# Kernel tuning notes

Hardware: AMD Instinct MI355X
Metric: run time of the kernel (lower is better)

The kernel has to match this reference:

```python
import jax, jax.numpy as jnp
import numpy as np

B_ = 2; L_ = 4096; D_MODEL = 1024; D_INNER = 2048; D_STATE = 128
N_HEADS = 32; HEADDIM = 64; D_CONV = 4; CHUNK = 64
CONV_DIM = D_INNER + 2 * D_STATE
EPS = 1e-5


def silu(x):
    return x * jax.nn.sigmoid(x)


def segsum(x):
    # x: (..., T) -> (..., T, T) stable segment sums; exp() gives 1-semiseparable matrix
    T = x.shape[-1]
    xe = jnp.broadcast_to(x[..., None], x.shape + (T,))  # (..., T, T)
    lower = jnp.tril(jnp.ones((T, T), bool), -1)
    xs = jnp.cumsum(jnp.where(lower, xe, 0.0), axis=-2)
    incl = jnp.tril(jnp.ones((T, T), bool), 0)
    return jnp.where(incl, xs, -jnp.inf)


def ssd(x, A, Bm, Cm):
    # x: (b, l, h, p); A: (b, l, h); Bm/Cm: (b, l, n) (single shared head, as in module)
    b, l, h, p = x.shape
    c = l // CHUNK
    x = x.reshape(b, c, CHUNK, h, p)
    A = A.reshape(b, c, CHUNK, h).transpose(0, 3, 1, 2)  # (b, h, c, l)
    Bm = Bm.reshape(b, c, CHUNK, D_STATE)
    Cm = Cm.reshape(b, c, CHUNK, D_STATE)
    A_cumsum = jnp.cumsum(A, axis=-1)                    # (b, h, c, l)
    Lmat = jnp.exp(segsum(A))                            # (b, h, c, l, l)
    # intra-chunk (diagonal blocks)
    Y_diag = jnp.einsum('bcln,bcsn,bhcls,bcshp->bclhp', Cm, Bm, Lmat, x)
    # per-chunk states
    decay_states = jnp.exp(A_cumsum[:, :, :, -1:] - A_cumsum)  # (b, h, c, l)
    states = jnp.einsum('bcln,bhcl,bclhp->bchpn', Bm, decay_states, x)
    init = jnp.zeros_like(states[:, :1])
    states = jnp.concatenate([init, states], axis=1)     # (b, c+1, h, p, n)
    A_last = jnp.pad(A_cumsum[:, :, :, -1], ((0, 0), (0, 0), (1, 0)))  # (b, h, c+1)
    decay_chunk = jnp.exp(segsum(A_last))                # (b, h, c+1, c+1)
    new_states = jnp.einsum('bhzc,bchpn->bzhpn', decay_chunk, states)
    states_prev = new_states[:, :-1]                     # (b, c, h, p, n)
    state_decay_out = jnp.exp(A_cumsum)
    Y_off = jnp.einsum('bcln,bchpn,bhcl->bclhp', Cm, states_prev, state_decay_out)
    return (Y_diag + Y_off).reshape(b, l, h, p)


def setup_inputs() -> dict:
    key = jax.random.key(0)
    ks = jax.random.split(key, 9)
    u = jax.random.normal(ks[0], (B_, L_, D_MODEL), jnp.float32)
    W_in = jax.random.normal(ks[1], (2 * D_INNER + 2 * D_STATE + N_HEADS, D_MODEL), jnp.float32) * (D_MODEL ** -0.5)
    conv_w = jax.random.normal(ks[2], (CONV_DIM, 1, D_CONV), jnp.float32) * 0.2
    conv_b = jax.random.normal(ks[3], (CONV_DIM,), jnp.float32) * 0.02
    dt_bias = jax.random.normal(ks[4], (N_HEADS,), jnp.float32) * 0.1
    A_log = jnp.log(jax.random.uniform(ks[5], (N_HEADS,), jnp.float32, 1.0, 16.0))
    D_param = jax.random.normal(ks[6], (N_HEADS,), jnp.float32) * 0.5
    norm_w = jnp.ones((D_INNER,), jnp.float32)
    W_out = jax.random.normal(ks[7], (D_MODEL, D_INNER), jnp.float32) * (D_INNER ** -0.5)
    return dict(u=u, W_in=W_in, conv_w=conv_w, conv_b=conv_b, dt_bias=dt_bias,
                A_log=A_log, D_param=D_param, norm_w=norm_w, W_out=W_out)


def mamba_forward(u, W_in, conv_w, conv_b, dt_bias, A_log, D_param, norm_w, W_out):
    b, l, _ = u.shape
    zxbcdt = u @ W_in.T                                  # (b, l, 2*di+2*ds+h)
    z = zxbcdt[..., :D_INNER]
    xBC = zxbcdt[..., D_INNER:D_INNER + CONV_DIM]
    dt = zxbcdt[..., D_INNER + CONV_DIM:]
    dt = jax.nn.softplus(dt + dt_bias)                   # (b, l, h)
    # causal depthwise conv1d
    xc = jnp.transpose(xBC, (0, 2, 1))                   # (b, conv_dim, l)
    xc = jax.lax.conv_general_dilated(xc, conv_w, (1,), [(D_CONV - 1, 0)],
                                      feature_group_count=CONV_DIM,
                                      dimension_numbers=('NCH', 'OIH', 'NCH'))
    xc = xc + conv_b[None, :, None]
    xBC = silu(jnp.transpose(xc, (0, 2, 1)))             # (b, l, conv_dim)
    x = xBC[..., :D_INNER]
    Bc = xBC[..., D_INNER:D_INNER + D_STATE]
    Cc = xBC[..., D_INNER + D_STATE:]
    x = x.reshape(b, l, N_HEADS, HEADDIM)
    A = -jnp.exp(A_log)                                  # (h,)
    Y = ssd(x * dt[..., None], A * dt, Bc, Cc)           # (b, l, h, p)
    y = Y + x * D_param[:, None]
    y = y.reshape(b, l, D_INNER)
    # gated RMSNorm
    y = y * silu(z)
    y = y * jax.lax.rsqrt(jnp.mean(y * y, axis=-1, keepdims=True) + EPS) * norm_w
    return y @ W_out.T


def reference(u, W_in, conv_w, conv_b, dt_bias, A_log, D_param, norm_w, W_out):
    return mamba_forward(u, W_in, conv_w, conv_b, dt_bias, A_log, D_param, norm_w, W_out)
```

## Files before the change

kernel.cpp:

```cpp
#include <hip/hip_runtime.h>
#include <hip/hip_bf16.h>
#include <math.h>

#define B_    2
#define L_    4096
#define DM    1024
#define DI    2048
#define DS    128
#define NH    32
#define HD    64
#define CHUNK 64
#define NC    (L_/CHUNK)
#define CD    (DI + 2*DS)
#define ROWS  (B_*L_)
#define NOUT  (2*DI + 2*DS + NH)
#define NPAD2 4608

typedef __attribute__((ext_vector_type(4))) float f32x4;
typedef __attribute__((ext_vector_type(8))) __bf16 bf16x8;
typedef __attribute__((ext_vector_type(4))) short s16x4;
typedef __attribute__((ext_vector_type(8))) short s16x8;

__global__ __launch_bounds__(256) void k_f32_to_bf16(const float* __restrict__ s, __bf16* __restrict__ d, int n4) {
    int i = blockIdx.x * 256 + threadIdx.x;
    if (i < n4) {
        f32x4 v = *(const f32x4*)(s + (size_t)i * 4);
        s16x4 o;
#pragma unroll
        for (int q = 0; q < 4; q++) o[q] = __builtin_bit_cast(short, (__bf16)v[q]);
        *(s16x4*)(d + (size_t)i * 4) = o;
    }
}

__global__ __launch_bounds__(256) void k_convert_pad(const float* __restrict__ s, __bf16* __restrict__ d, int nsrc4, int ndst4) {
    int i = blockIdx.x * 256 + threadIdx.x;
    if (i < ndst4) {
        s16x4 o = {0, 0, 0, 0};
        if (i < nsrc4) {
            f32x4 v = *(const f32x4*)(s + (size_t)i * 4);
#pragma unroll
            for (int q = 0; q < 4; q++) o[q] = __builtin_bit_cast(short, (__bf16)v[q]);
        }
        *(s16x4*)(d + (size_t)i * 4) = o;
    }
}

__device__ __forceinline__ void stage_half(const __bf16* __restrict__ G, int ldg, int grow0, int kt,
                                           char* lds, int ldsoff, int tid, int wave) {
#pragma unroll
    for (int issue = 0; issue < 2; issue++) {
        int o   = issue * 8192 + tid * 16;
        int row = o >> 7;
        int cb  = (o & 127) ^ ((row & 7) << 4);
        const __bf16* src = G + (size_t)(grow0 + row) * ldg + kt + (cb >> 1);
        char* ldsbase = lds + ldsoff + issue * 8192 + wave * 1024;
        __builtin_amdgcn_global_load_lds((const __attribute__((address_space(1))) void*)src,
                                         (__attribute__((address_space(3))) void*)ldsbase,
                                         16, 0, 0);
    }
}

__device__ __forceinline__ bf16x8 rdfrag(const char* lds, int ldsoff, int r, int ks, int lane) {
    int logical = r * 128 + ks * 64 + ((lane >> 4) << 4);
    int phys    = logical ^ ((r & 7) << 4);
    return *(const bf16x8*)(lds + ldsoff + phys);
}

#define MFMA_CLUSTER(AF, BF, ACC)                                                         \
    __builtin_amdgcn_s_setprio(1);                                                       \
    _Pragma("unroll")                                                                    \
    for (int fm = 0; fm < 4; fm++)                                                       \
        _Pragma("unroll")                                                                \
        for (int fn = 0; fn < 2; fn++)                                                   \
            _Pragma("unroll")                                                            \
            for (int ks = 0; ks < 2; ks++)                                               \
                ACC[fm][fn] = __builtin_amdgcn_mfma_f32_16x16x32_bf16(AF[fm][ks], BF[fn][ks], ACC[fm][fn], 0, 0, 0); \
    __builtin_amdgcn_s_setprio(0);

__device__ __forceinline__ void gemm256_core(const __bf16* __restrict__ Ag, const __bf16* __restrict__ Bg,
                                             int K, int m0, int n0, char* lds, f32x4 acc[4][4][2]) {
    const int tid = threadIdx.x, wave = tid >> 6, lane = tid & 63;
    const int wmq = wave >> 2, wnq = wave & 3, lrow = lane & 15;
    const int KT = K >> 6;
    auto Ahalf = [](int p, int mh) { return p * 65536 + mh * 16384; };
    auto Bhalf = [](int p, int nh) { return p * 65536 + 32768 + nh * 16384; };

    stage_half(Ag, K, m0,       0, lds, Ahalf(0, 0), tid, wave);
    stage_half(Bg, K, n0,       0, lds, Bhalf(0, 0), tid, wave);
    stage_half(Bg, K, n0 + 128, 0, lds, Bhalf(0, 1), tid, wave);
    stage_half(Ag, K, m0 + 128, 0, lds, Ahalf(0, 1), tid, wave);
    asm volatile("s_waitcnt vmcnt(0)" ::: "memory");
    __builtin_amdgcn_s_barrier();

    bf16x8 ra[4][2], rb[2][2], rb2[2][2];
#pragma unroll
    for (int fm = 0; fm < 4; fm++)
#pragma unroll
        for (int ks = 0; ks < 2; ks++)
            ra[fm][ks] = rdfrag(lds, Ahalf(0, 0), wmq * 64 + fm * 16 + lrow, ks, lane);
#pragma unroll
    for (int fn = 0; fn < 2; fn++)
#pragma unroll
        for (int ks = 0; ks < 2; ks++)
            rb[fn][ks] = rdfrag(lds, Bhalf(0, 0), wnq * 32 + fn * 16 + lrow, ks, lane);

    for (int t = 0; t < KT; t++) {
        const int p = t & 1, pn = p ^ 1, kn = (t + 1) << 6;
        const bool dsg = (t + 1 < KT);
        if (dsg) {
            stage_half(Ag, K, m0, kn, lds, Ahalf(pn, 0), tid, wave);
            stage_half(Bg, K, n0, kn, lds, Bhalf(pn, 0), tid, wave);
        }
#pragma unroll
        for (int fn = 0; fn < 2; fn++)
#pragma unroll
            for (int ks = 0; ks < 2; ks++)
                rb2[fn][ks] = rdfrag(lds, Bhalf(p, 1), wnq * 32 + fn * 16 + lrow, ks, lane);
        MFMA_CLUSTER(ra, rb, acc[0]);
        if (dsg) {
            stage_half(Bg, K, n0 + 128, kn, lds, Bhalf(pn, 1), tid, wave);
            stage_half(Ag, K, m0 + 128, kn, lds, Ahalf(pn, 1), tid, wave);
        }
        MFMA_CLUSTER(ra, rb2, acc[1]);
#pragma unroll
        for (int fm = 0; fm < 4; fm++)
#pragma unroll
            for (int ks = 0; ks < 2; ks++)
                ra[fm][ks] = rdfrag(lds, Ahalf(p, 1), wmq * 64 + fm * 16 + lrow, ks, lane);
        MFMA_CLUSTER(ra, rb2, acc[2]);
        MFMA_CLUSTER(ra, rb, acc[3]);
        asm volatile("s_waitcnt vmcnt(0)" ::: "memory");
        __builtin_amdgcn_s_barrier();
        if (dsg) {
#pragma unroll
            for (int fm = 0; fm < 4; fm++)
#pragma unroll
                for (int ks = 0; ks < 2; ks++)
                    ra[fm][ks] = rdfrag(lds, Ahalf(pn, 0), wmq * 64 + fm * 16 + lrow, ks, lane);
#pragma unroll
            for (int fn = 0; fn < 2; fn++)
#pragma unroll
                for (int ks = 0; ks < 2; ks++)
                    rb[fn][ks] = rdfrag(lds, Bhalf(pn, 0), wnq * 32 + fn * 16 + lrow, ks, lane);
        }
    }
}

__device__ __forceinline__ void gemm256x128_core(const __bf16* __restrict__ Ag, const __bf16* __restrict__ Bg,
                                                 int K, int m0, int n0, char* lds, f32x4 acc[8][2]) {
    const int tid = threadIdx.x, wave = tid >> 6, lane = tid & 63;
    const int wmq = wave >> 2, wnq = wave & 3, lrow = lane & 15;
    const int KT = K >> 6;
    const int aoff = wmq * 16384;

    auto stage_tile = [&](int t, int p) {
        const int kt = t << 6;
        stage_half(Ag, K, m0,       kt, lds, p * 49152,         tid, wave);
        stage_half(Ag, K, m0 + 128, kt, lds, p * 49152 + 16384, tid, wave);
        stage_half(Bg, K, n0,       kt, lds, p * 49152 + 32768, tid, wave);
    };
    stage_tile(0, 0);
    asm volatile("s_waitcnt vmcnt(0)" ::: "memory");
    __builtin_amdgcn_s_barrier();

    bf16x8 ra[4][2], rb[2][2];
#pragma unroll
    for (int fm = 0; fm < 4; fm++)
#pragma unroll
        for (int ks = 0; ks < 2; ks++)
            ra[fm][ks] = rdfrag(lds, aoff, fm * 16 + lrow, ks, lane);
#pragma unroll
    for (int fn = 0; fn < 2; fn++)
#pragma unroll
        for (int ks = 0; ks < 2; ks++)
            rb[fn][ks] = rdfrag(lds, 32768, wnq * 32 + fn * 16 + lrow, ks, lane);

    for (int t = 0; t < KT; t++) {
        const int p = t & 1, pn = p ^ 1;
        const bool dsg = (t + 1 < KT);
        if (dsg) {
            stage_half(Ag, K, m0,       (t + 1) << 6, lds, pn * 49152,         tid, wave);
            stage_half(Ag, K, m0 + 128, (t + 1) << 6, lds, pn * 49152 + 16384, tid, wave);
        }
        {
            f32x4 (*a0)[2] = &acc[0];
            MFMA_CLUSTER(ra, rb, a0);
        }
#pragma unroll
        for (int fm = 0; fm < 4; fm++)
#pragma unroll
            for (int ks = 0; ks < 2; ks++)
                ra[fm][ks] = rdfrag(lds, p * 49152 + aoff, 64 + fm * 16 + lrow, ks, lane);
        if (dsg) stage_half(Bg, K, n0, (t + 1) << 6, lds, pn * 49152 + 32768, tid, wave);
        {
            f32x4 (*a1)[2] = &acc[4];
            MFMA_CLUSTER(ra, rb, a1);
        }
        asm volatile("s_waitcnt vmcnt(0)" ::: "memory");
        __builtin_amdgcn_s_barrier();
        if (dsg) {
#pragma unroll
            for (int fm = 0; fm < 4; fm++)
#pragma unroll
                for (int ks = 0; ks < 2; ks++)
                    ra[fm][ks] = rdfrag(lds, pn * 49152 + aoff, fm * 16 + lrow, ks, lane);
#pragma unroll
            for (int fn = 0; fn < 2; fn++)
#pragma unroll
                for (int ks = 0; ks < 2; ks++)
                    rb[fn][ks] = rdfrag(lds, pn * 49152 + 32768, wnq * 32 + fn * 16 + lrow, ks, lane);
        }
    }
}

__global__ __launch_bounds__(512, 2) void k_gemm1(const __bf16* __restrict__ ubf, const __bf16* __restrict__ wibf,
                                                  __bf16* __restrict__ zbuf, __bf16* __restrict__ xbcraw,
                                                  float* __restrict__ dtbuf, const float* __restrict__ dt_bias) {
    extern __shared__ char lds[];
    f32x4 acc[4][4][2];
    f32x4 z4 = {0.f, 0.f, 0.f, 0.f};
#pragma unroll
    for (int q = 0; q < 4; q++)
#pragma unroll
        for (int i = 0; i < 4; i++)
#pragma unroll
            for (int j = 0; j < 2; j++) acc[q][i][j] = z4;

    int bid = blockIdx.x;
    int wg  = (bid & 7) * 72 + (bid >> 3);
    int m0  = (wg / 18) * 256;
    int n0  = (wg % 18) * 256;
    gemm256_core(ubf, wibf, DM, m0, n0, lds, acc);

    const int lane = threadIdx.x & 63, wave = threadIdx.x >> 6;
    const int wmq = wave >> 2, wnq = wave & 3;
#pragma unroll
    for (int q = 0; q < 4; q++) {
        const int mh = q >> 1, nh = (q & 1) ^ (q >> 1);
#pragma unroll
        for (int fm = 0; fm < 4; fm++) {
            const int gmb = m0 + mh * 128 + wmq * 64 + fm * 16 + ((lane >> 4) << 2);
#pragma unroll
            for (int fn = 0; fn < 2; fn++) {
                const int gn = n0 + nh * 128 + wnq * 32 + fn * 16 + (lane & 15);
                if (gn < DI) {
#pragma unroll
                    for (int r = 0; r < 4; r++)
                        zbuf[(size_t)(gmb + r) * DI + gn] = (__bf16)acc[q][fm][fn][r];
                } else if (gn < DI + CD) {
#pragma unroll
                    for (int r = 0; r < 4; r++)
                        xbcraw[(size_t)(gmb + r) * CD + (gn - DI)] = (__bf16)acc[q][fm][fn][r];
                } else if (gn < NOUT) {
                    const int hh = gn - (DI + CD);
                    const float bb = dt_bias[hh];
#pragma unroll
                    for (int r = 0; r < 4; r++) {
                        float x = acc[q][fm][fn][r] + bb;
                        float sp = (x > 20.f) ? x : log1pf(__expf(x));
                        dtbuf[(size_t)(gmb + r) * NH + hh] = sp;
                    }
                }
            }
        }
    }
}

__global__ __launch_bounds__(512, 2) void k_gemm2(const __bf16* __restrict__ ybf, const __bf16* __restrict__ wobf,
                                                  float* __restrict__ out) {
    extern __shared__ char lds[];
    f32x4 acc[8][2];
    f32x4 z4 = {0.f, 0.f, 0.f, 0.f};
#pragma unroll
    for (int i = 0; i < 8; i++)
#pragma unroll
        for (int j = 0; j < 2; j++) acc[i][j] = z4;

    int bid = blockIdx.x;
    int wg  = (bid & 7) * 32 + (bid >> 3);
    int m0  = (wg / 8) * 256;
    int n0  = (wg % 8) * 128;
    gemm256x128_core(ybf, wobf, DI, m0, n0, lds, acc);

    const int lane = threadIdx.x & 63, wave = threadIdx.x >> 6;
    const int wmq = wave >> 2, wnq = wave & 3;
#pragma unroll
    for (int fm = 0; fm < 8; fm++) {
        const int gmb = m0 + wmq * 128 + fm * 16 + ((lane >> 4) << 2);
#pragma unroll
        for (int fn = 0; fn < 2; fn++) {
            const int gn = n0 + wnq * 32 + fn * 16 + (lane & 15);
#pragma unroll
            for (int r = 0; r < 4; r++)
                out[(size_t)(gmb + r) * DM + gn] = acc[fm][fn][r];
        }
    }
}

__global__ __launch_bounds__(256) void k_conv(const __bf16* __restrict__ xbcraw, const float* __restrict__ conv_w,
                                              const float* __restrict__ conv_b, __bf16* __restrict__ xconv) {
    __shared__ float wsh[256 * 4];
    __shared__ float bsh[256];
    const int tid  = threadIdx.x;
    const int gsub = tid & 31;
    const int roct = tid >> 5;
    const int ch_base_blk = blockIdx.x * 256;
    *(f32x4*)&wsh[tid * 4] = *(const f32x4*)&conv_w[ch_base_blk * 4 + tid * 4];
    bsh[tid] = conv_b[ch_base_blk + tid];
    __syncthreads();

    const int ch0  = ch_base_blk + gsub * 8;
    const int row0 = (blockIdx.y * 8 + roct) * 8;
    const int l0   = row0 & (L_ - 1);
    const __bf16* src = xbcraw + (size_t)row0 * CD + ch0;

    s16x8 rr[11];
#pragma unroll
    for (int j = 0; j < 11; j++) {
        int ll = l0 - 3 + j;
        if (ll >= 0) rr[j] = *(const s16x8*)(src + (size_t)(j - 3) * CD);
        else         rr[j] = (s16x8){0, 0, 0, 0, 0, 0, 0, 0};
    }

    const int chl = gsub * 8;
    float w[8][4], bias[8];
#pragma unroll
    for (int j = 0; j < 8; j++) {
        bias[j] = bsh[chl + j];
#pragma unroll
        for (int k = 0; k < 4; k++) w[j][k] = wsh[(chl + j) * 4 + k];
    }

    __bf16* dst = xconv + (size_t)row0 * CD + ch0;
#pragma unroll
    for (int orow = 0; orow < 8; orow++) {
        float a[8];
#pragma unroll
        for (int j = 0; j < 8; j++) a[j] = bias[j];
#pragma unroll
        for (int k = 0; k < 4; k++) {
            s16x8 v = rr[orow + k];
#pragma unroll
            for (int j = 0; j < 8; j++)
                a[j] += w[j][k] * (float)__builtin_bit_cast(__bf16, (short)v[j]);
        }
        s16x8 o;
#pragma unroll
        for (int j = 0; j < 8; j++)
            o[j] = __builtin_bit_cast(short, (__bf16)(a[j] * __builtin_amdgcn_rcpf(1.f + __expf(-a[j]))));
        *(s16x8*)(dst + (size_t)orow * CD) = o;
    }
}

__global__ __launch_bounds__(256) void k_cbt(const __bf16* __restrict__ xconv, float* __restrict__ cbt) {
    const int c = blockIdx.x, b = blockIdx.y;
    const int tid = threadIdx.x, wv = tid >> 6, lane = tid & 63;
    const int lrow = lane & 15, lko = (lane >> 4) * 8;
    __shared__ __align__(16) __bf16 Csh[64 * 136];
    __shared__ __align__(16) __bf16 Bsh[64 * 136];
    const size_t rowbase = (size_t)b * L_ + c * CHUNK;
#pragma unroll
    for (int q = 0; q < 32; q++) {
        int i = q * 2 + (wv >> 1);
        int n = (wv & 1) * 64 + lane;
        const __bf16* base = xconv + (rowbase + i) * CD + DI;
        Bsh[i * 136 + n] = base[n];
        Csh[i * 136 + n] = base[DS + n];
    }
    __syncthreads();
    f32x4 acc[4];
    f32x4 z4 = {0.f, 0.f, 0.f, 0.f};
#pragma unroll
    for (int jt = 0; jt < 4; jt++) acc[jt] = z4;
#pragma unroll
    for (int ks = 0; ks < 4; ks++) {
        bf16x8 a = *(const bf16x8*)&Csh[(wv * 16 + lrow) * 136 + ks * 32 + lko];
#pragma unroll
        for (int jt = 0; jt < 4; jt++) {
            bf16x8 bb = *(const bf16x8*)&Bsh[(jt * 16 + lrow) * 136 + ks * 32 + lko];
            acc[jt] = __builtin_amdgcn_mfma_f32_16x16x32_bf16(a, bb, acc[jt], 0, 0, 0);
        }
    }
    float* o = cbt + (size_t)(b * NC + c) * 4096;
#pragma unroll
    for (int jt = 0; jt < 4; jt++)
#pragma unroll
        for (int r = 0; r < 4; r++) {
            int i = wv * 16 + (lane >> 4) * 4 + r;
            int j = jt * 16 + lrow;
            o[i * 64 + j] = acc[jt][r];
        }
}

__global__ __launch_bounds__(256) void k_ssd_a(const __bf16* __restrict__ xconv, const float* __restrict__ dtbuf,
                                               const float* __restrict__ cbt, const float* __restrict__ A_log,
                                               __bf16* __restrict__ ybuf, __bf16* __restrict__ states,
                                               float* __restrict__ asum, const float* __restrict__ D_param) {
    const int h = blockIdx.x, c = blockIdx.y, b = blockIdx.z;
    const int tid = threadIdx.x, wv = tid >> 6, lane = tid & 63;
    const int lrow = lane & 15, lko = (lane >> 4) * 8;
    __shared__ __align__(16) __bf16 xT[64 * 72];
    __shared__ __align__(16) __bf16 xsc[64 * 72];
    __shared__ __align__(16) __bf16 BT[128 * 72];
    __shared__ __align__(16) __bf16 Ms[64 * 72];
    __shared__ float dts[64], cum[64];

    const float Ah = -__expf(A_log[h]);
    const size_t rowbase = (size_t)b * L_ + c * CHUNK;

    float dtv = 0.f;
    if (wv == 0) { dtv = dtbuf[(rowbase + lane) * NH + h]; dts[lane] = dtv; }
#pragma unroll
    for (int q = 0; q < 16; q++) {
        int i = q * 4 + wv;
        xT[lane * 72 + i] = xconv[(rowbase + i) * CD + h * HD + lane];
    }
#pragma unroll
    for (int q = 0; q < 32; q++) {
        int i = q * 2 + (wv >> 1);
        int n = (wv & 1) * 64 + lane;
        BT[n * 72 + i] = xconv[(rowbase + i) * CD + DI + n];
    }
    if (wv == 0) {
        float v = Ah * dtv;
#pragma unroll
        for (int o = 1; o < 64; o <<= 1) { float t = __shfl_up(v, o); if (lane >= o) v += t; }
        cum[lane] = v;
        if (lane == 63) asum[(b * NC + c) * NH + h] = v;
    }
    __syncthreads();

    const float cum63 = cum[63];
    const float Dh = D_param[h];
    const float* cbt_bc = cbt + (size_t)(b * NC + c) * 4096;
#pragma unroll
    for (int q = 0; q < 16; q++) {
        int i = q * 4 + wv, j = lane;
        float cumi = cum[i];
        float m = 0.f;
        if (j <= i) m = cbt_bc[i * 64 + j] * __expf(cumi - cum[j]) * dts[j];
        if (j == i) m += Dh;
        Ms[i * 72 + j] = (__bf16)m;
        float dcfi = __expf(cum63 - cumi) * dts[i];
        xsc[lane * 72 + i] = (__bf16)((float)xT[lane * 72 + i] * dcfi);
    }
    __syncthreads();

    f32x4 z4 = {0.f, 0.f, 0.f, 0.f};
    {
        f32x4 accY[4];
#pragma unroll
        for (int pt = 0; pt < 4; pt++) accY[pt] = z4;
#pragma unroll
        for (int ks = 0; ks < 2; ks++) {
            bf16x8 a = *(const bf16x8*)&Ms[(wv * 16 + lrow) * 72 + ks * 32 + lko];
#pragma unroll
            for (int pt = 0; pt < 4; pt++) {
                bf16x8 bb = *(const bf16x8*)&xT[(pt * 16 + lrow) * 72 + ks * 32 + lko];
                accY[pt] = __builtin_amdgcn_mfma_f32_16x16x32_bf16(a, bb, accY[pt], 0, 0, 0);
            }
        }
#pragma unroll
        for (int pt = 0; pt < 4; pt++)
#pragma unroll
            for (int r = 0; r < 4; r++) {
                int i = wv * 16 + (lane >> 4) * 4 + r;
                int p = pt * 16 + lrow;
                ybuf[(rowbase + i) * DI + h * HD + p] = (__bf16)accY[pt][r];
            }
    }
    {
        f32x4 accS[8];
#pragma unroll
        for (int nt = 0; nt < 8; nt++) accS[nt] = z4;
#pragma unroll
        for (int ks = 0; ks < 2; ks++) {
            bf16x8 a = *(const bf16x8*)&xsc[(wv * 16 + lrow) * 72 + ks * 32 + lko];
#pragma unroll
            for (int nt = 0; nt < 8; nt++) {
                bf16x8 bb = *(const bf16x8*)&BT[(nt * 16 + lrow) * 72 + ks * 32 + lko];
                accS[nt] = __builtin_amdgcn_mfma_f32_16x16x32_bf16(a, bb, accS[nt], 0, 0, 0);
            }
        }
        __bf16* sp = states + ((size_t)(b * NC + c) * NH + h) * 8192;
#pragma unroll
        for (int nt = 0; nt < 8; nt++)
#pragma unroll
            for (int r = 0; r < 4; r++) {
                int p = wv * 16 + (lane >> 4) * 4 + r;
                int n = nt * 16 + lrow;
                sp[p * 128 + n] = (__bf16)accS[nt][r];
            }
    }
}

__global__ __launch_bounds__(256) void k_scan(__bf16* __restrict__ states, const float* __restrict__ asum) {
    const int seg = blockIdx.x, h = blockIdx.y, b = blockIdx.z;
    __shared__ float efs[NC];
    if (threadIdx.x < NC) efs[threadIdx.x] = __expf(asum[(b * NC + threadIdx.x) * NH + h]);
    __syncthreads();
    const int e0 = seg * 1024 + threadIdx.x * 4;
    __bf16* base = states + ((size_t)(b * NC) * NH + h) * 8192 + e0;
    const size_t cs = (size_t)NH * 8192;
    float S[4] = {0.f, 0.f, 0.f, 0.f};
    s16x4 r0 = *(const s16x4*)(base);
    s16x4 r1 = *(const s16x4*)(base + cs);
    s16x4 r2 = *(const s16x4*)(base + 2 * cs);
    s16x4 r3;
#define SCAN_STEP(RV, CC)                                                                  \
    {                                                                                      \
        s16x4 o; float e = efs[CC];                                                        \
        _Pragma("unroll")                                                                  \
        for (int q = 0; q < 4; q++) {                                                      \
            float t = (float)__builtin_bit_cast(__bf16, (short)RV[q]);                     \
            o[q] = __builtin_bit_cast(short, (__bf16)S[q]);                                \
            S[q] = e * S[q] + t;                                                           \
        }                                                                                  \
        *(s16x4*)(base + (size_t)(CC) * cs) = o;                                           \
    }
    for (int c = 0; c < NC; c += 4) {
        r3 = *(const s16x4*)(base + (size_t)(c + 3) * cs);
        SCAN_STEP(r0, c);
        if (c + 4 < NC) r0 = *(const s16x4*)(base + (size_t)(c + 4) * cs);
        SCAN_STEP(r1, c + 1);
        if (c + 5 < NC) r1 = *(const s16x4*)(base + (size_t)(c + 5) * cs);
        SCAN_STEP(r2, c + 2);
        if (c + 6 < NC) r2 = *(const s16x4*)(base + (size_t)(c + 6) * cs);
        SCAN_STEP(r3, c + 3);
    }
#undef SCAN_STEP
}

__global__ __launch_bounds__(256) void k_ssd_b(const __bf16* __restrict__ xconv, const float* __restrict__ dtbuf,
                                               const __bf16* __restrict__ states, const float* __restrict__ A_log,
                                               __bf16* __restrict__ ybuf) {
    const int h = blockIdx.x, c = blockIdx.y, b = blockIdx.z;
    const int tid = threadIdx.x, wv = tid >> 6, lane = tid & 63;
    const int lrow = lane & 15, lko = (lane >> 4) * 8;
    __shared__ __align__(16) __bf16 Csh[64 * 136];
    __shared__ __align__(16) __bf16 Sps[64 * 136];
    __shared__ float cum[64];

    const float Ah = -__expf(A_log[h]);
    const size_t rowbase = (size_t)b * L_ + c * CHUNK;
    const __bf16* sp = states + ((size_t)(b * NC + c) * NH + h) * 8192;
#pragma unroll
    for (int q = 0; q < 32; q++) {
        int i = q * 2 + (wv >> 1);
        int n = (wv & 1) * 64 + lane;
        Csh[i * 136 + n] = xconv[(rowbase + i) * CD + DI + DS + n];
        Sps[i * 136 + n] = sp[i * 128 + n];
    }
    if (wv == 0) {
        float v = Ah * dtbuf[(rowbase + lane) * NH + h];
#pragma unroll
        for (int o = 1; o < 64; o <<= 1) { float t = __shfl_up(v, o); if (lane >= o) v += t; }
        cum[lane] = v;
    }
    __syncthreads();

    f32x4 acc[4];
    f32x4 z4 = {0.f, 0.f, 0.f, 0.f};
#pragma unroll
    for (int pt = 0; pt < 4; pt++) acc[pt] = z4;
#pragma unroll
    for (int ks = 0; ks < 4; ks++) {
        bf16x8 a = *(const bf16x8*)&Csh[(wv * 16 + lrow) * 136 + ks * 32 + lko];
#pragma unroll
        for (int pt = 0; pt < 4; pt++) {
            bf16x8 bb = *(const bf16x8*)&Sps[(pt * 16 + lrow) * 136 + ks * 32 + lko];
            acc[pt] = __builtin_amdgcn_mfma_f32_16x16x32_bf16(a, bb, acc[pt], 0, 0, 0);
        }
    }
#pragma unroll
    for (int r = 0; r < 4; r++) {
        int i = wv * 16 + (lane >> 4) * 4 + r;
        float ef = __expf(cum[i]);
#pragma unroll
        for (int pt = 0; pt < 4; pt++) {
            size_t idx = (rowbase + i) * DI + h * HD + pt * 16 + lrow;
            float y0 = (float)ybuf[idx];
            ybuf[idx] = (__bf16)(y0 + ef * acc[pt][r]);
        }
    }
}

__global__ __launch_bounds__(256) void k_gate_norm(const __bf16* __restrict__ ybuf, const __bf16* __restrict__ zbuf,
                                                   const float* __restrict__ norm_w, __bf16* __restrict__ ybf) {
    const int r = blockIdx.x;
    const int tid = threadIdx.x;
    const int col0 = tid * 8;
    s16x8 y8 = *(const s16x8*)(ybuf + (size_t)r * DI + col0);
    s16x8 z8 = *(const s16x8*)(zbuf + (size_t)r * DI + col0);
    float v[8];
    float ss = 0.f;
#pragma unroll
    for (int q = 0; q < 8; q++) {
        float y = (float)__builtin_bit_cast(__bf16, (short)y8[q]);
        float z = (float)__builtin_bit_cast(__bf16, (short)z8[q]);
        float g = z * __builtin_amdgcn_rcpf(1.f + __expf(-z));
        v[q] = y * g;
        ss += v[q] * v[q];
    }
#pragma unroll
    for (int o = 32; o > 0; o >>= 1) ss += __shfl_down(ss, o);
    __shared__ float wsum[4];
    __shared__ float rmss;
    if ((tid & 63) == 0) wsum[tid >> 6] = ss;
    __syncthreads();
    if (tid == 0) {
        float t = wsum[0] + wsum[1] + wsum[2] + wsum[3];
        rmss = rsqrtf(t / (float)DI + 1e-5f);
    }
    __syncthreads();
    float rm = rmss;
    s16x8 o8;
#pragma unroll
    for (int q = 0; q < 8; q++)
        o8[q] = __builtin_bit_cast(short, (__bf16)(v[q] * rm * norm_w[col0 + q]));
    *(s16x8*)(ybf + (size_t)r * DI + col0) = o8;
}

extern "C" void kernel_launch(void* const* d_in, const int* in_sizes, int n_in,
                              void* d_out, int out_size, void* d_ws, size_t ws_size,
                              hipStream_t stream) {
    const float* u       = (const float*)d_in[0];
    const float* W_in    = (const float*)d_in[1];
    const float* conv_w  = (const float*)d_in[2];
    const float* conv_b  = (const float*)d_in[3];
    const float* dt_bias = (const float*)d_in[4];
    const float* A_log   = (const float*)d_in[5];
    const float* D_param = (const float*)d_in[6];
    const float* norm_w  = (const float*)d_in[7];
    const float* W_out   = (const float*)d_in[8];
    float* out = (float*)d_out;

    constexpr size_t OFF_WOBF  = 0;
    constexpr size_t OFF_ZBUF  = 4194304;
    constexpr size_t OFF_DT    = 37748736;
    constexpr size_t OFF_ASUM  = 38797312;
    constexpr size_t OFF_XCONV = 38813696;
    constexpr size_t OFF_CBT   = 76562432;
    constexpr size_t OFF_BIG   = 78659584;
    constexpr size_t NEED      = 145768448;
    if (ws_size < NEED) return;

    char* ws = (char*)d_ws;
    __bf16* wobf   = (__bf16*)(ws + OFF_WOBF);
    __bf16* zbuf   = (__bf16*)(ws + OFF_ZBUF);
    float*  dtbuf  = (float*) (ws + OFF_DT);
    float*  asum   = (float*) (ws + OFF_ASUM);
    __bf16* xconv  = (__bf16*)(ws + OFF_XCONV);
    float*  cbt    = (float*) (ws + OFF_CBT);
    __bf16* ubf    = (__bf16*)(ws + OFF_BIG);
    __bf16* wibf   = (__bf16*)(ws + OFF_BIG + 16777216);
    __bf16* xbcraw = (__bf16*)(ws + OFF_BIG + 16777216 + 9437184);
    __bf16* states = (__bf16*)(ws + OFF_BIG);
    __bf16* ybf    = (__bf16*)(ws + OFF_XCONV);
    __bf16* ybuf   = (__bf16*)d_out;

    (void)hipFuncSetAttribute((const void*)k_gemm1, hipFuncAttributeMaxDynamicSharedMemorySize, 131072);
    (void)hipFuncSetAttribute((const void*)k_gemm2, hipFuncAttributeMaxDynamicSharedMemorySize, 98304);

    k_f32_to_bf16<<<(ROWS * DM / 4 + 255) / 256, 256, 0, stream>>>(u, ubf, ROWS * DM / 4);
    k_convert_pad<<<(NPAD2 * DM / 4 + 255) / 256, 256, 0, stream>>>(W_in, wibf, NOUT * DM / 4, NPAD2 * DM / 4);
    k_f32_to_bf16<<<(DM * DI / 4 + 255) / 256, 256, 0, stream>>>(W_out, wobf, DM * DI / 4);

    k_gemm1<<<576, 512, 131072, stream>>>(ubf, wibf, zbuf, xbcraw, dtbuf, dt_bias);
    k_conv<<<dim3(9, 128), 256, 0, stream>>>(xbcraw, conv_w, conv_b, xconv);
    k_cbt<<<dim3(NC, B_), 256, 0, stream>>>(xconv, cbt);
    k_ssd_a<<<dim3(NH, NC, B_), 256, 0, stream>>>(xconv, dtbuf, cbt, A_log, ybuf, states, asum, D_param);
    k_scan<<<dim3(8, NH, B_), 256, 0, stream>>>(states, asum);
    k_ssd_b<<<dim3(NH, NC, B_), 256, 0, stream>>>(xconv, dtbuf, states, A_log, ybuf);
    k_gate_norm<<<ROWS, 256, 0, stream>>>(ybuf, zbuf, norm_w, ybf);
    k_gemm2<<<256, 512, 98304, stream>>>(ybf, wobf, out);
}
```

Measured before the change: 311.2 us.

## Rewrite in-projection GEMM main loop as an 8-phase ping-pong schedule

Replaces the double-buffered 256x256 GEMM core used by the input projection with an 8-phase schedule. Each phase interleaves LDS fragment reads, one global-to-LDS stage of a half tile, and one MFMA cluster, separated by barriers and partial vmcnt waits. Two K tiles are kept in flight, and the accumulator quadrant mapping changes to match. The aim is to spread memory traffic evenly across MFMA work and hide load latency, at the cost of many more barriers per K step.

```diff
diff --git a/kernel.cpp b/kernel.cpp
--- a/kernel.cpp
+++ b/kernel.cpp
@@ -77,73 +77,66 @@
                 ACC[fm][fn] = __builtin_amdgcn_mfma_f32_16x16x32_bf16(AF[fm][ks], BF[fn][ks], ACC[fm][fn], 0, 0, 0); \
     __builtin_amdgcn_s_setprio(0);
 
-__device__ __forceinline__ void gemm256_core(const __bf16* __restrict__ Ag, const __bf16* __restrict__ Bg,
-                                             int K, int m0, int n0, char* lds, f32x4 acc[4][4][2]) {
+#define RDA(SET, BUF, H)                                                                  \
+    _Pragma("unroll") for (int fm = 0; fm < 4; fm++)                                      \
+    _Pragma("unroll") for (int ks = 0; ks < 2; ks++)                                      \
+        SET[fm][ks] = rdfrag(lds, (BUF)*65536 + (H)*16384, wmq*64 + fm*16 + lrow, ks, lane);
+#define RDB(SET, BUF, H)                                                                  \
+    _Pragma("unroll") for (int fn = 0; fn < 2; fn++)                                      \
+    _Pragma("unroll") for (int ks = 0; ks < 2; ks++)                                      \
+        SET[fn][ks] = rdfrag(lds, (BUF)*65536 + 32768 + (H)*16384, wnq*32 + fn*16 + lrow, ks, lane);
+#define STA(BUF, H, KOFF) stage_half(Ag, K, m0 + (H)*128, (KOFF), lds, (BUF)*65536 + (H)*16384, tid, wave)
+#define STB(BUF, H, KOFF) stage_half(Bg, K, n0 + (H)*128, (KOFF), lds, (BUF)*65536 + 32768 + (H)*16384, tid, wave)
+#define BAR() __builtin_amdgcn_s_barrier()
+#define LGKM0() asm volatile("s_waitcnt lgkmcnt(0)" ::: "memory")
+#define VMW(N) asm volatile("s_waitcnt vmcnt(" #N ")" ::: "memory")
+
+__device__ __forceinline__ void gemm256_8ph(const __bf16* __restrict__ Ag, const __bf16* __restrict__ Bg,
+                                            int K, int m0, int n0, char* lds, f32x4 acc[4][4][2]) {
     const int tid = threadIdx.x, wave = tid >> 6, lane = tid & 63;
     const int wmq = wave >> 2, wnq = wave & 3, lrow = lane & 15;
     const int KT = K >> 6;
-    auto Ahalf = [](int p, int mh) { return p * 65536 + mh * 16384; };
-    auto Bhalf = [](int p, int nh) { return p * 65536 + 32768 + nh * 16384; };
-
-    stage_half(Ag, K, m0,       0, lds, Ahalf(0, 0), tid, wave);
-    stage_half(Bg, K, n0,       0, lds, Bhalf(0, 0), tid, wave);
-    stage_half(Bg, K, n0 + 128, 0, lds, Bhalf(0, 1), tid, wave);
-    stage_half(Ag, K, m0 + 128, 0, lds, Ahalf(0, 1), tid, wave);
-    asm volatile("s_waitcnt vmcnt(0)" ::: "memory");
-    __builtin_amdgcn_s_barrier();
-
-    bf16x8 ra[4][2], rb[2][2], rb2[2][2];
-#pragma unroll
-    for (int fm = 0; fm < 4; fm++)
-#pragma unroll
-        for (int ks = 0; ks < 2; ks++)
-            ra[fm][ks] = rdfrag(lds, Ahalf(0, 0), wmq * 64 + fm * 16 + lrow, ks, lane);
-#pragma unroll
-    for (int fn = 0; fn < 2; fn++)
-#pragma unroll
-        for (int ks = 0; ks < 2; ks++)
-            rb[fn][ks] = rdfrag(lds, Bhalf(0, 0), wnq * 32 + fn * 16 + lrow, ks, lane);
-
-    for (int t = 0; t < KT; t++) {
-        const int p = t & 1, pn = p ^ 1, kn = (t + 1) << 6;
-        const bool dsg = (t + 1 < KT);
-        if (dsg) {
-            stage_half(Ag, K, m0, kn, lds, Ahalf(pn, 0), tid, wave);
-            stage_half(Bg, K, n0, kn, lds, Bhalf(pn, 0), tid, wave);
-        }
-#pragma unroll
-        for (int fn = 0; fn < 2; fn++)
-#pragma unroll
-            for (int ks = 0; ks < 2; ks++)
-                rb2[fn][ks] = rdfrag(lds, Bhalf(p, 1), wnq * 32 + fn * 16 + lrow, ks, lane);
-        MFMA_CLUSTER(ra, rb, acc[0]);
-        if (dsg) {
-            stage_half(Bg, K, n0 + 128, kn, lds, Bhalf(pn, 1), tid, wave);
-            stage_half(Ag, K, m0 + 128, kn, lds, Ahalf(pn, 1), tid, wave);
-        }
-        MFMA_CLUSTER(ra, rb2, acc[1]);
-#pragma unroll
-        for (int fm = 0; fm < 4; fm++)
-#pragma unroll
-            for (int ks = 0; ks < 2; ks++)
-                ra[fm][ks] = rdfrag(lds, Ahalf(p, 1), wmq * 64 + fm * 16 + lrow, ks, lane);
-        MFMA_CLUSTER(ra, rb2, acc[2]);
-        MFMA_CLUSTER(ra, rb, acc[3]);
-        asm volatile("s_waitcnt vmcnt(0)" ::: "memory");
-        __builtin_amdgcn_s_barrier();
-        if (dsg) {
-#pragma unroll
-            for (int fm = 0; fm < 4; fm++)
-#pragma unroll
-                for (int ks = 0; ks < 2; ks++)
-                    ra[fm][ks] = rdfrag(lds, Ahalf(pn, 0), wmq * 64 + fm * 16 + lrow, ks, lane);
-#pragma unroll
-            for (int fn = 0; fn < 2; fn++)
-#pragma unroll
-                for (int ks = 0; ks < 2; ks++)
-                    rb[fn][ks] = rdfrag(lds, Bhalf(pn, 0), wnq * 32 + fn * 16 + lrow, ks, lane);
-        }
-    }
+    const int NB = (KT >> 1) - 1;
+
+    bf16x8 a0s[4][2], a1s[4][2], b0s[2][2], b1s[2][2];
+
+    STA(0, 0, 0);  STB(0, 0, 0);  STA(0, 1, 0);  STB(0, 1, 0);
+    STA(1, 0, 64); STB(1, 0, 64); STA(1, 1, 64); STB(1, 1, 64);
+    VMW(8); BAR();
+    RDA(a0s, 0, 0); RDB(b0s, 0, 0);
+    BAR(); LGKM0(); MFMA_CLUSTER(a0s, b0s, acc[2]); BAR();
+    RDA(a1s, 0, 1);
+    BAR(); LGKM0(); MFMA_CLUSTER(a1s, b0s, acc[3]); BAR();
+
+    for (int i = 0; i < NB; i++) {
+        const int k2 = (2 * i + 2) << 6, k3 = k2 + 64;
+        RDB(b1s, 0, 1); STB(0, 0, k2);
+        BAR(); LGKM0(); MFMA_CLUSTER(a0s, b1s, acc[0]); BAR();
+        STA(0, 0, k2);
+        BAR(); LGKM0(); MFMA_CLUSTER(a1s, b1s, acc[1]); VMW(4); BAR();
+        RDA(a0s, 1, 0); RDB(b0s, 1, 0); STA(0, 1, k2);
+        BAR(); LGKM0(); MFMA_CLUSTER(a0s, b0s, acc[2]); BAR();
+        RDA(a1s, 1, 1); STB(0, 1, k2);
+        BAR(); LGKM0(); MFMA_CLUSTER(a1s, b0s, acc[3]); BAR();
+        RDB(b1s, 1, 1); STB(1, 0, k3);
+        BAR(); LGKM0(); MFMA_CLUSTER(a0s, b1s, acc[0]); BAR();
+        STA(1, 0, k3);
+        BAR(); LGKM0(); MFMA_CLUSTER(a1s, b1s, acc[1]); VMW(4); BAR();
+        RDA(a0s, 0, 0); RDB(b0s, 0, 0); STA(1, 1, k3);
+        BAR(); LGKM0(); MFMA_CLUSTER(a0s, b0s, acc[2]); BAR();
+        RDA(a1s, 0, 1); STB(1, 1, k3);
+        BAR(); LGKM0(); MFMA_CLUSTER(a1s, b0s, acc[3]); BAR();
+    }
+    RDB(b1s, 0, 1);
+    BAR(); LGKM0(); MFMA_CLUSTER(a0s, b1s, acc[0]); BAR();
+    BAR(); LGKM0(); MFMA_CLUSTER(a1s, b1s, acc[1]); VMW(0); BAR();
+    RDA(a0s, 1, 0); RDB(b0s, 1, 0);
+    BAR(); LGKM0(); MFMA_CLUSTER(a0s, b0s, acc[2]); BAR();
+    RDA(a1s, 1, 1);
+    BAR(); LGKM0(); MFMA_CLUSTER(a1s, b0s, acc[3]); BAR();
+    RDB(b1s, 1, 1);
+    BAR(); LGKM0(); MFMA_CLUSTER(a0s, b1s, acc[0]); BAR();
+    LGKM0(); MFMA_CLUSTER(a1s, b1s, acc[1]);
 }
 
 __device__ __forceinline__ void gemm256x128_core(const __bf16* __restrict__ Ag, const __bf16* __restrict__ Bg,
@@ -230,13 +223,13 @@
     int wg  = (bid & 7) * 72 + (bid >> 3);
     int m0  = (wg / 18) * 256;
     int n0  = (wg % 18) * 256;
-    gemm256_core(ubf, wibf, DM, m0, n0, lds, acc);
+    gemm256_8ph(ubf, wibf, DM, m0, n0, lds, acc);
 
     const int lane = threadIdx.x & 63, wave = threadIdx.x >> 6;
     const int wmq = wave >> 2, wnq = wave & 3;
 #pragma unroll
-    for (int q = 0; q < 4; q++) {
-        const int mh = q >> 1, nh = (q & 1) ^ (q >> 1);
+    for (int j = 0; j < 4; j++) {
+        const int mh = j & 1, nh = 1 - (j >> 1);
 #pragma unroll
         for (int fm = 0; fm < 4; fm++) {
             const int gmb = m0 + mh * 128 + wmq * 64 + fm * 16 + ((lane >> 4) << 2);
@@ -246,17 +239,17 @@
                 if (gn < DI) {
 #pragma unroll
                     for (int r = 0; r < 4; r++)
-                        zbuf[(size_t)(gmb + r) * DI + gn] = (__bf16)acc[q][fm][fn][r];
+                        zbuf[(size_t)(gmb + r) * DI + gn] = (__bf16)acc[j][fm][fn][r];
                 } else if (gn < DI + CD) {
 #pragma unroll
                     for (int r = 0; r < 4; r++)
-                        xbcraw[(size_t)(gmb + r) * CD + (gn - DI)] = (__bf16)acc[q][fm][fn][r];
+                        xbcraw[(size_t)(gmb + r) * CD + (gn - DI)] = (__bf16)acc[j][fm][fn][r];
                 } else if (gn < NOUT) {
                     const int hh = gn - (DI + CD);
                     const float bb = dt_bias[hh];
 #pragma unroll
                     for (int r = 0; r < 4; r++) {
-                        float x = acc[q][fm][fn][r] + bb;
+                        float x = acc[j][fm][fn][r] + bb;
                         float sp = (x > 20.f) ? x : log1pf(__expf(x));
                         dtbuf[(size_t)(gmb + r) * NH + hh] = sp;
                     }
```

Result: slower. 475.2 us (+52.7%).

## Shrink gemm1 tile to 128x256 with single-buffered LDS and higher occupancy

Applied to the files above, without the earlier changes.

Replaces the double-buffered, software-pipelined 256x256 gemm1 core with a simpler single-buffered 128x256 tile. LDS use per block drops from 128KB to 48KB and the launch bound goes from 2 to 4 blocks per CU, so twice as many workgroups run with more resident per CU. The aim is to hide load latency through occupancy instead of explicit prefetch. The trade is that global loads are no longer overlapped with MFMA inside a block, each block now has two barriers per K step, and the smaller M tile gives less reuse of the B operand.

```diff
diff --git a/kernel.cpp b/kernel.cpp
--- a/kernel.cpp
+++ b/kernel.cpp
@@ -77,72 +77,41 @@
                 ACC[fm][fn] = __builtin_amdgcn_mfma_f32_16x16x32_bf16(AF[fm][ks], BF[fn][ks], ACC[fm][fn], 0, 0, 0); \
     __builtin_amdgcn_s_setprio(0);
 
-__device__ __forceinline__ void gemm256_core(const __bf16* __restrict__ Ag, const __bf16* __restrict__ Bg,
-                                             int K, int m0, int n0, char* lds, f32x4 acc[4][4][2]) {
+__device__ __forceinline__ void gemm128x256_core(const __bf16* __restrict__ Ag, const __bf16* __restrict__ Bg,
+                                                 int K, int m0, int n0, char* lds, f32x4 acc[4][4]) {
     const int tid = threadIdx.x, wave = tid >> 6, lane = tid & 63;
-    const int wmq = wave >> 2, wnq = wave & 3, lrow = lane & 15;
+    const int wm = wave >> 2, wn = wave & 3, lrow = lane & 15;
     const int KT = K >> 6;
-    auto Ahalf = [](int p, int mh) { return p * 65536 + mh * 16384; };
-    auto Bhalf = [](int p, int nh) { return p * 65536 + 32768 + nh * 16384; };
-
-    stage_half(Ag, K, m0,       0, lds, Ahalf(0, 0), tid, wave);
-    stage_half(Bg, K, n0,       0, lds, Bhalf(0, 0), tid, wave);
-    stage_half(Bg, K, n0 + 128, 0, lds, Bhalf(0, 1), tid, wave);
-    stage_half(Ag, K, m0 + 128, 0, lds, Ahalf(0, 1), tid, wave);
-    asm volatile("s_waitcnt vmcnt(0)" ::: "memory");
-    __builtin_amdgcn_s_barrier();
-
-    bf16x8 ra[4][2], rb[2][2], rb2[2][2];
-#pragma unroll
-    for (int fm = 0; fm < 4; fm++)
-#pragma unroll
-        for (int ks = 0; ks < 2; ks++)
-            ra[fm][ks] = rdfrag(lds, Ahalf(0, 0), wmq * 64 + fm * 16 + lrow, ks, lane);
-#pragma unroll
-    for (int fn = 0; fn < 2; fn++)
-#pragma unroll
-        for (int ks = 0; ks < 2; ks++)
-            rb[fn][ks] = rdfrag(lds, Bhalf(0, 0), wnq * 32 + fn * 16 + lrow, ks, lane);
+    const int brow = wn * 64;
+    const int bhalf = 16384 + ((brow >> 7) << 14);
+    const int brl = brow & 127;
 
     for (int t = 0; t < KT; t++) {
-        const int p = t & 1, pn = p ^ 1, kn = (t + 1) << 6;
-        const bool dsg = (t + 1 < KT);
-        if (dsg) {
-            stage_half(Ag, K, m0, kn, lds, Ahalf(pn, 0), tid, wave);
-            stage_half(Bg, K, n0, kn, lds, Bhalf(pn, 0), tid, wave);
-        }
-#pragma unroll
-        for (int fn = 0; fn < 2; fn++)
-#pragma unroll
-            for (int ks = 0; ks < 2; ks++)
-                rb2[fn][ks] = rdfrag(lds, Bhalf(p, 1), wnq * 32 + fn * 16 + lrow, ks, lane);
-        MFMA_CLUSTER(ra, rb, acc[0]);
-        if (dsg) {
-            stage_half(Bg, K, n0 + 128, kn, lds, Bhalf(pn, 1), tid, wave);
-            stage_half(Ag, K, m0 + 128, kn, lds, Ahalf(pn, 1), tid, wave);
-        }
-        MFMA_CLUSTER(ra, rb2, acc[1]);
-#pragma unroll
-        for (int fm = 0; fm < 4; fm++)
-#pragma unroll
-            for (int ks = 0; ks < 2; ks++)
-                ra[fm][ks] = rdfrag(lds, Ahalf(p, 1), wmq * 64 + fm * 16 + lrow, ks, lane);
-        MFMA_CLUSTER(ra, rb2, acc[2]);
-        MFMA_CLUSTER(ra, rb, acc[3]);
+        const int kt = t << 6;
+        stage_half(Ag, K, m0,       kt, lds, 0,     tid, wave);
+        stage_half(Bg, K, n0,       kt, lds, 16384, tid, wave);
+        stage_half(Bg, K, n0 + 128, kt, lds, 32768, tid, wave);
         asm volatile("s_waitcnt vmcnt(0)" ::: "memory");
         __builtin_amdgcn_s_barrier();
-        if (dsg) {
-#pragma unroll
-            for (int fm = 0; fm < 4; fm++)
-#pragma unroll
-                for (int ks = 0; ks < 2; ks++)
-                    ra[fm][ks] = rdfrag(lds, Ahalf(pn, 0), wmq * 64 + fm * 16 + lrow, ks, lane);
-#pragma unroll
-            for (int fn = 0; fn < 2; fn++)
-#pragma unroll
-                for (int ks = 0; ks < 2; ks++)
-                    rb[fn][ks] = rdfrag(lds, Bhalf(pn, 0), wnq * 32 + fn * 16 + lrow, ks, lane);
-        }
+        bf16x8 a[4][2];
+#pragma unroll
+        for (int fm = 0; fm < 4; fm++)
+#pragma unroll
+            for (int ks = 0; ks < 2; ks++)
+                a[fm][ks] = rdfrag(lds, 0, wm * 64 + fm * 16 + lrow, ks, lane);
+        __builtin_amdgcn_s_setprio(1);
+#pragma unroll
+        for (int fn = 0; fn < 4; fn++) {
+            bf16x8 b0 = rdfrag(lds, bhalf, brl + fn * 16 + lrow, 0, lane);
+            bf16x8 b1 = rdfrag(lds, bhalf, brl + fn * 16 + lrow, 1, lane);
+#pragma unroll
+            for (int fm = 0; fm < 4; fm++) {
+                acc[fm][fn] = __builtin_amdgcn_mfma_f32_16x16x32_bf16(a[fm][0], b0, acc[fm][fn], 0, 0, 0);
+                acc[fm][fn] = __builtin_amdgcn_mfma_f32_16x16x32_bf16(a[fm][1], b1, acc[fm][fn], 0, 0, 0);
+            }
+        }
+        __builtin_amdgcn_s_setprio(0);
+        __builtin_amdgcn_s_barrier();
     }
 }
 
@@ -213,53 +182,49 @@
     }
 }
 
-__global__ __launch_bounds__(512, 2) void k_gemm1(const __bf16* __restrict__ ubf, const __bf16* __restrict__ wibf,
+__global__ __launch_bounds__(512, 4) void k_gemm1(const __bf16* __restrict__ ubf, const __bf16* __restrict__ wibf,
                                                   __bf16* __restrict__ zbuf, __bf16* __restrict__ xbcraw,
                                                   float* __restrict__ dtbuf, const float* __restrict__ dt_bias) {
     extern __shared__ char lds[];
-    f32x4 acc[4][4][2];
+    f32x4 acc[4][4];
     f32x4 z4 = {0.f, 0.f, 0.f, 0.f};
 #pragma unroll
-    for (int q = 0; q < 4; q++)
-#pragma unroll
-        for (int i = 0; i < 4; i++)
-#pragma unroll
-            for (int j = 0; j < 2; j++) acc[q][i][j] = z4;
+    for (int i = 0; i < 4; i++)
+#pragma unroll
+        for (int j = 0; j < 4; j++) acc[i][j] = z4;
 
     int bid = blockIdx.x;
-    int wg  = (bid & 7) * 72 + (bid >> 3);
-    int m0  = (wg / 18) * 256;
+    int wg  = (bid & 7) * 144 + (bid >> 3);
+    int m0  = (wg / 18) * 128;
     int n0  = (wg % 18) * 256;
-    gemm256_core(ubf, wibf, DM, m0, n0, lds, acc);
+    gemm128x256_core(ubf, wibf, DM, m0, n0, lds, acc);
 
     const int lane = threadIdx.x & 63, wave = threadIdx.x >> 6;
-    const int wmq = wave >> 2, wnq = wave & 3;
-#pragma unroll
-    for (int q = 0; q < 4; q++) {
-        const int mh = q >> 1, nh = (q & 1) ^ (q >> 1);
-#pragma unroll
-        for (int fm = 0; fm < 4; fm++) {
-            const int gmb = m0 + mh * 128 + wmq * 64 + fm * 16 + ((lane >> 4) << 2);
-#pragma unroll
-            for (int fn = 0; fn < 2; fn++) {
-                const int gn = n0 + nh * 128 + wnq * 32 + fn * 16 + (lane & 15);
-                if (gn < DI) {
-#pragma unroll
-                    for (int r = 0; r < 4; r++)
-                        zbuf[(size_t)(gmb + r) * DI + gn] = (__bf16)acc[q][fm][fn][r];
-                } else if (gn < DI + CD) {
-#pragma unroll
-                    for (int r = 0; r < 4; r++)
-                        xbcraw[(size_t)(gmb + r) * CD + (gn - DI)] = (__bf16)acc[q][fm][fn][r];
-                } else if (gn < NOUT) {
-                    const int hh = gn - (DI + CD);
-                    const float bb = dt_bias[hh];
-#pragma unroll
-                    for (int r = 0; r < 4; r++) {
-                        float x = acc[q][fm][fn][r] + bb;
-                        float sp = (x > 20.f) ? x : log1pf(__expf(x));
-                        dtbuf[(size_t)(gmb + r) * NH + hh] = sp;
-                    }
+    const int wm = wave >> 2, wn = wave & 3;
+    const int gm_base = m0 + wm * 64 + ((lane >> 4) << 2);
+    const int gn_base = n0 + wn * 64 + (lane & 15);
+#pragma unroll
+    for (int fm = 0; fm < 4; fm++) {
+        const int gmb = gm_base + fm * 16;
+#pragma unroll
+        for (int fn = 0; fn < 4; fn++) {
+            const int gn = gn_base + fn * 16;
+            if (gn < DI) {
+#pragma unroll
+                for (int r = 0; r < 4; r++)
+                    zbuf[(size_t)(gmb + r) * DI + gn] = (__bf16)acc[fm][fn][r];
+            } else if (gn < DI + CD) {
+#pragma unroll
+                for (int r = 0; r < 4; r++)
+                    xbcraw[(size_t)(gmb + r) * CD + (gn - DI)] = (__bf16)acc[fm][fn][r];
+            } else if (gn < NOUT) {
+                const int hh = gn - (DI + CD);
+                const float bb = dt_bias[hh];
+#pragma unroll
+                for (int r = 0; r < 4; r++) {
+                    float x = acc[fm][fn][r] + bb;
+                    float sp = (x > 20.f) ? x : log1pf(__expf(x));
+                    dtbuf[(size_t)(gmb + r) * NH + hh] = sp;
                 }
             }
         }
@@ -659,14 +624,14 @@
     __bf16* ybf    = (__bf16*)(ws + OFF_XCONV);
     __bf16* ybuf   = (__bf16*)d_out;
 
-    (void)hipFuncSetAttribute((const void*)k_gemm1, hipFuncAttributeMaxDynamicSharedMemorySize, 131072);
+    (void)hipFuncSetAttribute((const void*)k_gemm1, hipFuncAttributeMaxDynamicSharedMemorySize, 49152);
     (void)hipFuncSetAttribute((const void*)k_gemm2, hipFuncAttributeMaxDynamicSharedMemorySize, 98304);
 
     k_f32_to_bf16<<<(ROWS * DM / 4 + 255) / 256, 256, 0, stream>>>(u, ubf, ROWS * DM / 4);
     k_convert_pad<<<(NPAD2 * DM / 4 + 255) / 256, 256, 0, stream>>>(W_in, wibf, NOUT * DM / 4, NPAD2 * DM / 4);
     k_f32_to_bf16<<<(DM * DI / 4 + 255) / 256, 256, 0, stream>>>(W_out, wobf, DM * DI / 4);
 
-    k_gemm1<<<576, 512, 131072, stream>>>(ubf, wibf, zbuf, xbcraw, dtbuf, dt_bias);
+    k_gemm1<<<1152, 512, 49152, stream>>>(ubf, wibf, zbuf, xbcraw, dtbuf, dt_bias);
     k_conv<<<dim3(9, 128), 256, 0, stream>>>(xbcraw, conv_w, conv_b, xconv);
     k_cbt<<<dim3(NC, B_), 256, 0, stream>>>(xconv, cbt);
     k_ssd_a<<<dim3(NH, NC, B_), 256, 0, stream>>>(xconv, dtbuf, cbt, A_log, ybuf, states, asum, D_param);
```

Result: no change. 308.7 us (-0.8%).
